# Optimization experiments

Hardware: AMD Instinct MI355X
Metric: run time of the kernel (lower is better)

The kernel has to match this reference:

```python
import jax, jax.numpy as jnp
import numpy as np

KERNEL_SIZES = [1, 2, 3]
KERNEL_NUM = 11
SIGMA = 0.1
EXACT_SIGMA = 0.001
EMBED_DIM = 300
HIDDEN = 128
Q_VOCAB = 30000
D_VOCAB = 30000


def _mus_sigmas():
    mus, sigmas = [], []
    K = KERNEL_NUM
    for i in range(K):
        mu = 1.0 / (K - 1) + 2.0 * i / (K - 1) - 1.0
        sigma = SIGMA
        if mu > 1.0:
            sigma = EXACT_SIGMA
            mu = 1.0
        mus.append(mu)
        sigmas.append(sigma)
    return jnp.asarray(mus, jnp.float32), jnp.asarray(sigmas, jnp.float32)


def _conv_tanh(x_bcl, w, b, ks):
    # x_bcl: (B, C_in, L); ConstantPad1d((0, ks)) + Conv1d(kernel=ks+1) keeps length L
    y = jax.lax.conv_general_dilated(
        x_bcl, w, window_strides=(1,), padding=[(0, ks)],
        dimension_numbers=('NCW', 'OIW', 'NCW'))
    return jnp.tanh(y + b[None, :, None])  # (B, H, L)


def _l2norm(x):
    n = jnp.sqrt(jnp.sum(x * x, axis=-1, keepdims=True))
    return x / jnp.maximum(n, 1e-12)


def setup_inputs() -> dict:
    key = jax.random.key(0)
    ks = jax.random.split(key, 16)
    inp = {
        'query': jax.random.randint(ks[0], (128, 128), 0, Q_VOCAB),
        'doc': jax.random.randint(ks[1], (128, 512), 0, D_VOCAB),
        'q_emb': jax.random.normal(ks[2], (Q_VOCAB, EMBED_DIM), jnp.float32) * 0.1,
        'd_emb': jax.random.normal(ks[3], (D_VOCAB, EMBED_DIM), jnp.float32) * 0.1,
        'out_w': jax.random.normal(ks[4], (1, 3 * 3 * KERNEL_NUM), jnp.float32) * 0.1,
        'out_b': jnp.zeros((1,), jnp.float32),
    }
    for idx, k in enumerate(KERNEL_SIZES):
        fan_in = EMBED_DIM * (k + 1)
        inp[f'conv_w{idx}'] = jax.random.normal(ks[5 + 2 * idx], (HIDDEN, EMBED_DIM, k + 1), jnp.float32) / np.sqrt(fan_in)
        inp[f'conv_b{idx}'] = jnp.zeros((HIDDEN,), jnp.float32)
    return inp


def reference(query, doc, q_emb, d_emb, conv_w0, conv_b0, conv_w1, conv_b1,
              conv_w2, conv_b2, out_w, out_b):
    mus, sigmas = _mus_sigmas()
    inv2s2 = 1.0 / (2.0 * sigmas * sigmas)  # (K,)

    q_e = q_emb[query].transpose(0, 2, 1)  # (B, D, Lq)
    d_e = d_emb[doc].transpose(0, 2, 1)    # (B, D, Ld)

    cws = [(conv_w0, conv_b0), (conv_w1, conv_b1), (conv_w2, conv_b2)]
    # q_convs/d_convs share weights (same nn.Sequential appended to both lists)
    q_convs = [_l2norm(_conv_tanh(q_e, w, b, ks).transpose(0, 2, 1))
               for (w, b), ks in zip(cws, KERNEL_SIZES)]  # each (B, Lq, H)
    d_convs = [_l2norm(_conv_tanh(d_e, w, b, ks).transpose(0, 2, 1))
               for (w, b), ks in zip(cws, KERNEL_SIZES)]  # each (B, Ld, H)

    KM = []
    for qi in range(3):
        for di in range(3):
            mm = jnp.einsum('bld,brd->blr', q_convs[qi], d_convs[di])  # (B,Lq,Ld)
            # Gaussian kernel soft-histogram, vectorized over all kernels
            kern = jnp.exp(-(mm[..., None] - mus) ** 2 * inv2s2)  # (B,Lq,Ld,K)
            K = jnp.log1p(kern.sum(axis=2)).sum(axis=1)           # (B,K)
            KM.append(K)
    phi = jnp.concatenate(KM, axis=1)  # (B, 9*KERNEL_NUM)
    return phi @ out_w.T + out_b       # (B, 1)
```

## Files before the change

### kernel.cpp

```cpp
#include <hip/hip_runtime.h>
#include <hip/hip_bf16.h>

typedef __hip_bfloat16 bf16;
typedef __attribute__((ext_vector_type(8))) short short8;
typedef __attribute__((ext_vector_type(4))) float f32x4;
typedef __attribute__((ext_vector_type(2))) float f32x2;

#define NB 128
#define NH 128
#define NLQ 128
#define NLD 512
#define NEMB 300
#define XQROWS 132
#define XDROWS 516
#define XCOLS 320

__device__ __forceinline__ unsigned short bfbits(float x) {
    __hip_bfloat16 h = __float2bfloat16(x);
    return *reinterpret_cast<unsigned short*>(&h);
}

__device__ __forceinline__ float fast_tanh(float x) {
    x = fminf(9.f, fmaxf(-9.f, x));
    float e = __builtin_amdgcn_exp2f(x * 2.8853900817779268f);
    return (e - 1.f) * __builtin_amdgcn_rcpf(e + 1.f);
}

__global__ void pack_w(const float* __restrict__ cw0, const float* __restrict__ cw1,
                       const float* __restrict__ cw2, bf16* __restrict__ Wp)
{
    int widx = blockIdx.y;
    int W = widx + 2;
    int e = blockIdx.x * 256 + threadIdx.x;
    if (e >= W * 40960) return;
    int ch = e >> 12;
    int cc = ch / W;
    int t  = ch - cc * W;
    int h  = (e >> 5) & 127;
    int cp = e & 31;
    int c  = cc * 32 + cp;
    const float* cw = (widx == 0) ? cw0 : (widx == 1 ? cw1 : cw2);
    float v = (c < NEMB) ? cw[(h * NEMB + c) * W + t] : 0.f;
    size_t off = (widx == 0) ? 0 : (widx == 1 ? 81920 : 204800);
    Wp[off + e] = __float2bfloat16(v);
}

__global__ __launch_bounds__(256)
void pack_x(const int* __restrict__ q_tok, const int* __restrict__ d_tok,
            const float* __restrict__ q_emb, const float* __restrict__ d_emb,
            bf16* __restrict__ Xq, bf16* __restrict__ Xd)
{
    int gid = blockIdx.x * 256 + threadIdx.x;
    int row = gid / 20, g = gid - row * 20;
    const float* emb; bf16* dst; int tok;
    if (row < NB * XQROWS) {
        int b = row / XQROWS, l = row - b * XQROWS;
        tok = (l < NLQ) ? q_tok[b * NLQ + l] : -1;
        emb = q_emb;
        dst = Xq + (size_t)row * XCOLS + g * 16;
    } else {
        int rowd = row - NB * XQROWS;
        int b = rowd / XDROWS, l = rowd - b * XDROWS;
        tok = (l < NLD) ? d_tok[b * NLD + l] : -1;
        emb = d_emb;
        dst = Xd + (size_t)rowd * XCOLS + g * 16;
    }
    int c0 = g * 16;
    float4 v[4];
    #pragma unroll
    for (int q = 0; q < 4; ++q) {
        int c = c0 + q * 4;
        v[q] = make_float4(0.f, 0.f, 0.f, 0.f);
        if (tok >= 0 && c < NEMB)
            v[q] = *reinterpret_cast<const float4*>(emb + (size_t)tok * NEMB + c);
    }
    short8 o0, o1;
    o0[0] = (short)bfbits(v[0].x); o0[1] = (short)bfbits(v[0].y);
    o0[2] = (short)bfbits(v[0].z); o0[3] = (short)bfbits(v[0].w);
    o0[4] = (short)bfbits(v[1].x); o0[5] = (short)bfbits(v[1].y);
    o0[6] = (short)bfbits(v[1].z); o0[7] = (short)bfbits(v[1].w);
    o1[0] = (short)bfbits(v[2].x); o1[1] = (short)bfbits(v[2].y);
    o1[2] = (short)bfbits(v[2].z); o1[3] = (short)bfbits(v[2].w);
    o1[4] = (short)bfbits(v[3].x); o1[5] = (short)bfbits(v[3].y);
    o1[6] = (short)bfbits(v[3].z); o1[7] = (short)bfbits(v[3].w);
    *reinterpret_cast<short8*>(dst) = o0;
    *reinterpret_cast<short8*>(dst + 8) = o1;
}

__global__ __launch_bounds__(512, 4)
void conv_kernel(const bf16* __restrict__ Xq, const bf16* __restrict__ Xd,
                 const bf16* __restrict__ Wp,
                 const float* __restrict__ cb0, const float* __restrict__ cb1,
                 const float* __restrict__ cb2,
                 bf16* __restrict__ qn, bf16* __restrict__ dn)
{
    __shared__ bf16 Xs[2][132][40];
    __shared__ float ssq[2][256];

    int bx = blockIdx.x;
    int widx = bx % 3;
    int inner = bx / 3;
    int W = widx + 2;
    const bf16* wp = Wp + ((widx == 0) ? 0 : (widx == 1 ? 81920 : 204800));
    const float* cb = (widx == 0) ? cb0 : (widx == 1 ? cb1 : cb2);

    int tid = threadIdx.x;
    int lane = tid & 63;
    int wv = tid >> 6;
    int wr = wv >> 1;
    int wc = wv & 1;
    int s_wave = wr >> 1;
    int lr_base = (wr & 1) * 64;

    bf16* outp; int L;
    int sb0, sb1, sl00, sl01;
    const bf16* xbase;
    size_t grow0, grow1;
    if (inner < 64) {
        outp = qn + (size_t)widx * NB * NLQ * NH;
        L = NLQ; sb0 = inner * 2; sb1 = sb0 + 1; sl00 = 0; sl01 = 0;
        xbase = Xq; grow0 = (size_t)sb0 * XQROWS; grow1 = (size_t)sb1 * XQROWS;
    } else {
        int i = inner - 64;
        outp = dn + (size_t)widx * NB * NLD * NH;
        L = NLD; sb0 = i >> 1; sb1 = sb0; sl00 = (i & 1) * 256; sl01 = sl00 + 128;
        xbase = Xd; grow0 = (size_t)sb0 * XDROWS + sl00; grow1 = grow0 + 128;
    }

    int sr = tid >> 2;
    int colg = tid & 3;
    const bf16* gsrc0 = xbase + (grow0 + sr) * XCOLS + colg * 8;
    const bf16* gsrc1 = xbase + (grow1 + sr) * XCOLS + colg * 8;
    bf16* ld0 = &Xs[0][sr][colg * 8];
    bf16* ld1 = &Xs[1][sr][colg * 8];
    bool has_tail = (tid >= 448 && tid < 480);
    int j = tid - 448;
    int ts = (j >> 2) >> 2, trr = 128 + ((j >> 2) & 3), tcolg = j & 3;
    const bf16* gsrcT = xbase + ((ts ? grow1 : grow0) + trr) * XCOLS + tcolg * 8;
    bf16* ldT = &Xs[ts][trr][tcolg * 8];

    short8 a0, a1, at;
    a0 = *reinterpret_cast<const short8*>(gsrc0);
    a1 = *reinterpret_cast<const short8*>(gsrc1);
    if (has_tail) at = *reinterpret_cast<const short8*>(gsrcT);
    *reinterpret_cast<short8*>(ld0) = a0;
    *reinterpret_cast<short8*>(ld1) = a1;
    if (has_tail) *reinterpret_cast<short8*>(ldT) = at;
    __syncthreads();

    f32x4 acc[4][4];
    #pragma unroll
    for (int m = 0; m < 4; ++m)
        #pragma unroll
        for (int n = 0; n < 4; ++n)
            acc[m][n] = (f32x4){0.f, 0.f, 0.f, 0.f};

    const bf16* pB = wp + ((size_t)((wc * 64 + (lane & 15)) * 4 + (lane >> 4))) * 8;

    int step = 0;
    for (int cc = 0; cc < 10; ++cc) {
        if (cc < 9) {
            a0 = *reinterpret_cast<const short8*>(gsrc0 + (cc + 1) * 32);
            a1 = *reinterpret_cast<const short8*>(gsrc1 + (cc + 1) * 32);
            if (has_tail) at = *reinterpret_cast<const short8*>(gsrcT + (cc + 1) * 32);
        }
        for (int t = 0; t < W; ++t, ++step) {
            const bf16* pBs = pB + (size_t)step * 4096;
            short8 bv[4], af[4];
            #pragma unroll
            for (int n = 0; n < 4; ++n)
                bv[n] = *reinterpret_cast<const short8*>(pBs + n * 512);
            #pragma unroll
            for (int m = 0; m < 4; ++m)
                af[m] = *reinterpret_cast<const short8*>(
                    &Xs[s_wave][lr_base + m * 16 + (lane & 15) + t][(lane >> 4) * 8]);
            #pragma unroll
            for (int m = 0; m < 4; ++m)
                #pragma unroll
                for (int n = 0; n < 4; ++n)
                    acc[m][n] = __builtin_amdgcn_mfma_f32_16x16x32_bf16(af[m], bv[n], acc[m][n], 0, 0, 0);
        }
        if (cc < 9) {
            __syncthreads();
            *reinterpret_cast<short8*>(ld0) = a0;
            *reinterpret_cast<short8*>(ld1) = a1;
            if (has_tail) *reinterpret_cast<short8*>(ldT) = at;
            __syncthreads();
        }
    }

    float ssl[4][4];
    #pragma unroll
    for (int m = 0; m < 4; ++m)
        #pragma unroll
        for (int i = 0; i < 4; ++i) ssl[m][i] = 0.f;

    #pragma unroll
    for (int n = 0; n < 4; ++n) {
        float bias = cb[wc * 64 + n * 16 + (lane & 15)];
        #pragma unroll
        for (int m = 0; m < 4; ++m)
            #pragma unroll
            for (int i = 0; i < 4; ++i) {
                float v = fast_tanh(acc[m][n][i] + bias);
                acc[m][n][i] = v;
                ssl[m][i] += v * v;
            }
    }
    #pragma unroll
    for (int m = 0; m < 4; ++m)
        #pragma unroll
        for (int i = 0; i < 4; ++i) {
            float s = ssl[m][i];
            s += __shfl_xor(s, 1); s += __shfl_xor(s, 2);
            s += __shfl_xor(s, 4); s += __shfl_xor(s, 8);
            ssl[m][i] = s;
        }
    if ((lane & 15) == 0) {
        #pragma unroll
        for (int m = 0; m < 4; ++m)
            #pragma unroll
            for (int i = 0; i < 4; ++i)
                ssq[wc][wr * 64 + m * 16 + (lane >> 4) * 4 + i] = ssl[m][i];
    }
    __syncthreads();
    #pragma unroll
    for (int m = 0; m < 4; ++m)
        #pragma unroll
        for (int i = 0; i < 4; ++i) {
            int r = wr * 64 + m * 16 + (lane >> 4) * 4 + i;
            float s2 = ssq[0][r] + ssq[1][r];
            float sc = 1.f / fmaxf(sqrtf(s2), 1e-12f);
            int s = r >> 7, lr = r & 127;
            int b = s ? sb1 : sb0;
            int l = (s ? sl01 : sl00) + lr;
            bf16* dst = outp + ((size_t)(b * L + l)) * NH;
            #pragma unroll
            for (int n = 0; n < 4; ++n)
                dst[wc * 64 + n * 16 + (lane & 15)] = __float2bfloat16(acc[m][n][i] * sc);
        }
}

__global__ __launch_bounds__(512, 4)
void sim_kernel(const bf16* __restrict__ qn, const bf16* __restrict__ dn,
                float* __restrict__ phi)
{
    __shared__ bf16 Qs[128][136];
    __shared__ bf16 Ds[64][136];
    __shared__ float wsum[2][11];
    float (*red)[128][11] = reinterpret_cast<float(*)[128][11]>(&Ds[0][0]);

    int blk = blockIdx.x;
    int b = blk / 9;
    int pair = blk - b * 9;
    int qi = pair / 3, di = pair - qi * 3;

    int tid = threadIdx.x, lane = tid & 63, wv = tid >> 6;
    int wr = wv >> 2;
    int wc = wv & 3;

    const bf16* qbase = qn + ((size_t)qi * NB + b) * (NLQ * NH);
    const bf16* dbase = dn + ((size_t)di * NB + b) * (NLD * NH);

    {
        int r = tid >> 2, h0 = (tid & 3) * 32;
        #pragma unroll
        for (int v = 0; v < 4; ++v)
            *reinterpret_cast<short8*>(&Qs[r][h0 + v * 8]) =
                *reinterpret_cast<const short8*>(qbase + (size_t)r * NH + h0 + v * 8);
    }

    int dr = tid >> 3, dc = (tid & 7) * 16;
    {
        short8 st[2];
        #pragma unroll
        for (int v = 0; v < 2; ++v)
            st[v] = *reinterpret_cast<const short8*>(dbase + (size_t)dr * NH + dc + v * 8);
        #pragma unroll
        for (int v = 0; v < 2; ++v)
            *reinterpret_cast<short8*>(&Ds[dr][dc + v * 8]) = st[v];
    }
    __syncthreads();

    f32x2 sums2[2][11];
    #pragma unroll
    for (int n = 0; n < 2; ++n)
        #pragma unroll
        for (int k = 0; k < 11; ++k) sums2[n][k] = (f32x2){0.f, 0.f};

    const float C1 = 1.8315638888734179e-2f;
    const float C2 = 3.3546262790251185e-4f;
    const float C3 = 6.1442123533282098e-6f;
    const float C4 = 1.1253517471925912e-7f;

    for (int cc = 0; cc < 8; ++cc) {
        f32x4 acc[2][2];
        #pragma unroll
        for (int m = 0; m < 2; ++m)
            #pragma unroll
            for (int n = 0; n < 2; ++n)
                acc[m][n] = (f32x4){0.f, 0.f, 0.f, 0.f};

        #pragma unroll
        for (int kc = 0; kc < 4; ++kc) {
            short8 af[2], bq[2];
            #pragma unroll
            for (int m = 0; m < 2; ++m)
                af[m] = *reinterpret_cast<const short8*>(
                    &Ds[wr * 32 + m * 16 + (lane & 15)][kc * 32 + (lane >> 4) * 8]);
            #pragma unroll
            for (int n = 0; n < 2; ++n)
                bq[n] = *reinterpret_cast<const short8*>(
                    &Qs[wc * 32 + n * 16 + (lane & 15)][kc * 32 + (lane >> 4) * 8]);
            #pragma unroll
            for (int m = 0; m < 2; ++m)
                #pragma unroll
                for (int n = 0; n < 2; ++n)
                    acc[m][n] = __builtin_amdgcn_mfma_f32_16x16x32_bf16(af[m], bq[n], acc[m][n], 0, 0, 0);
        }
        __syncthreads();

        short8 st[2];
        if (cc < 7) {
            #pragma unroll
            for (int v = 0; v < 2; ++v)
                st[v] = *reinterpret_cast<const short8*>(
                    dbase + (size_t)((cc + 1) * 64 + dr) * NH + dc + v * 8);
        }

        #pragma unroll
        for (int n = 0; n < 2; ++n)
            #pragma unroll
            for (int i = 0; i < 4; ++i) {
                f32x2 x2;
                x2.x = acc[0][n][i];
                x2.y = acc[1][n][i];
                f32x2 ax = x2 * 28.853900817779268f;
                f32x2 R, Ri, E4;
                R.x = __builtin_amdgcn_exp2f(ax.x);
                R.y = __builtin_amdgcn_exp2f(ax.y);
                Ri.x = __builtin_amdgcn_rcpf(R.x);
                Ri.y = __builtin_amdgcn_rcpf(R.y);
                f32x2 d4 = x2 + 0.1f;
                f32x2 t = d4 * d4 * (-72.134752044448169f);
                E4.x = __builtin_amdgcn_exp2f(t.x);
                E4.y = __builtin_amdgcn_exp2f(t.y);
                sums2[n][4] += E4;
                f32x2 u = E4 * R;
                sums2[n][5] += u;
                u *= R; u *= C1; sums2[n][6] += u;
                u *= R; u *= C2; sums2[n][7] += u;
                u *= R; u *= C3; sums2[n][8] += u;
                u *= R; u *= C4; sums2[n][9] += u;
                f32x2 w = E4 * Ri; w *= C1; sums2[n][3] += w;
                w *= Ri; w *= C2; sums2[n][2] += w;
                w *= Ri; w *= C3; sums2[n][1] += w;
                w *= Ri; w *= C4; sums2[n][0] += w;
                if (__any(fmaxf(x2.x, x2.y) > 0.98f)) {
                    f32x2 d1 = x2 - 1.0f;
                    f32x2 t1 = d1 * d1 * (-721347.52044448f);
                    f32x2 e;
                    e.x = __builtin_amdgcn_exp2f(t1.x);
                    e.y = __builtin_amdgcn_exp2f(t1.y);
                    sums2[n][10] += e;
                }
            }

        if (cc < 7) {
            #pragma unroll
            for (int v = 0; v < 2; ++v)
                *reinterpret_cast<short8*>(&Ds[dr][dc + v * 8]) = st[v];
            __syncthreads();
        }
    }

    #pragma unroll
    for (int n = 0; n < 2; ++n)
        #pragma unroll
        for (int k = 0; k < 11; ++k) {
            float s = sums2[n][k].x + sums2[n][k].y;
            s += __shfl_xor(s, 16);
            s += __shfl_xor(s, 32);
            sums2[n][k].x = s;
        }
    if ((lane >> 4) == 0) {
        #pragma unroll
        for (int n = 0; n < 2; ++n)
            #pragma unroll
            for (int k = 0; k < 11; ++k)
                red[wr][wc * 32 + n * 16 + (lane & 15)][k] = sums2[n][k].x;
    }
    __syncthreads();
    if (tid < 128) {
        float lv[11];
        #pragma unroll
        for (int k = 0; k < 11; ++k)
            lv[k] = log1pf(red[0][tid][k] + red[1][tid][k]);
        #pragma unroll
        for (int k = 0; k < 11; ++k) {
            float s = lv[k];
            s += __shfl_xor(s, 1); s += __shfl_xor(s, 2); s += __shfl_xor(s, 4);
            s += __shfl_xor(s, 8); s += __shfl_xor(s, 16); s += __shfl_xor(s, 32);
            lv[k] = s;
        }
        if ((tid & 63) == 0) {
            #pragma unroll
            for (int k = 0; k < 11; ++k) wsum[tid >> 6][k] = lv[k];
        }
    }
    __syncthreads();
    if (tid < 11) phi[b * 99 + pair * 11 + tid] = wsum[0][tid] + wsum[1][tid];
}

__global__ void final_kernel(const float* __restrict__ phi, const float* __restrict__ ow,
                             const float* __restrict__ obias, float* __restrict__ out)
{
    int b = threadIdx.x;
    float s = obias[0];
    #pragma unroll
    for (int j = 0; j < 99; ++j) s += phi[b * 99 + j] * ow[j];
    out[b] = s;
}

extern "C" void kernel_launch(void* const* d_in, const int* in_sizes, int n_in,
                              void* d_out, int out_size, void* d_ws, size_t ws_size,
                              hipStream_t stream)
{
    const int*   query = (const int*)d_in[0];
    const int*   doc   = (const int*)d_in[1];
    const float* q_emb = (const float*)d_in[2];
    const float* d_emb = (const float*)d_in[3];
    const float* out_w = (const float*)d_in[4];
    const float* out_b = (const float*)d_in[5];
    const float* cw0 = (const float*)d_in[6];
    const float* cb0 = (const float*)d_in[7];
    const float* cw1 = (const float*)d_in[8];
    const float* cb1 = (const float*)d_in[9];
    const float* cw2 = (const float*)d_in[10];
    const float* cb2 = (const float*)d_in[11];

    const size_t QN = (size_t)NB * NLQ * NH;
    const size_t DN = (size_t)NB * NLD * NH;
    const size_t XQN = (size_t)NB * XQROWS * XCOLS;
    const size_t XDN = (size_t)NB * XDROWS * XCOLS;

    bf16* Wp = (bf16*)d_ws;
    bf16* Xq = Wp + 368640;
    bf16* Xd = Xq + XQN;
    bf16* qn = Xd + XDN;
    bf16* dn = qn + 3 * QN;
    float* phi = (float*)(dn + 3 * DN);

    pack_w<<<dim3(640, 3), 256, 0, stream>>>(cw0, cw1, cw2, Wp);
    pack_x<<<6480, 256, 0, stream>>>(query, doc, q_emb, d_emb, Xq, Xd);
    conv_kernel<<<960, 512, 0, stream>>>(Xq, Xd, Wp, cb0, cb1, cb2, qn, dn);
    sim_kernel<<<NB * 9, 512, 0, stream>>>(qn, dn, phi);
    final_kernel<<<1, 128, 0, stream>>>(phi, out_w, out_b, (float*)d_out);
}
```

Measured before the change: 227.9 us.

## Double-buffer conv LDS tile and template conv body on kernel width

The conv kernel now keeps two LDS buffers for the input tile, so the next chunk is written into the alternate buffer and only one barrier per chunk is needed instead of two. The body is also templated on the window width, which lets the inner tap loop fully unroll with compile-time weight offsets. The cost is doubled LDS per block, which may lower the number of resident blocks per CU. An extra barrier protects the ssq reduction buffer.

```diff
diff --git a/kernel.cpp b/kernel.cpp
--- a/kernel.cpp
+++ b/kernel.cpp
@@ -87,23 +87,13 @@
     *reinterpret_cast<short8*>(dst + 8) = o1;
 }
 
-__global__ __launch_bounds__(512, 4)
-void conv_kernel(const bf16* __restrict__ Xq, const bf16* __restrict__ Xd,
-                 const bf16* __restrict__ Wp,
-                 const float* __restrict__ cb0, const float* __restrict__ cb1,
-                 const float* __restrict__ cb2,
-                 bf16* __restrict__ qn, bf16* __restrict__ dn)
-{
-    __shared__ bf16 Xs[2][132][40];
-    __shared__ float ssq[2][256];
-
-    int bx = blockIdx.x;
-    int widx = bx % 3;
-    int inner = bx / 3;
-    int W = widx + 2;
-    const bf16* wp = Wp + ((widx == 0) ? 0 : (widx == 1 ? 81920 : 204800));
-    const float* cb = (widx == 0) ? cb0 : (widx == 1 ? cb1 : cb2);
-
+template<int W>
+__device__ __forceinline__ void conv_body(
+    const bf16* __restrict__ Xq, const bf16* __restrict__ Xd,
+    const bf16* __restrict__ wp, const float* __restrict__ cb,
+    bf16* __restrict__ qn_w, bf16* __restrict__ dn_w,
+    int inner, bf16 Xs[2][2][132][40], float ssq[2][256])
+{
     int tid = threadIdx.x;
     int lane = tid & 63;
     int wv = tid >> 6;
@@ -117,12 +107,12 @@
     const bf16* xbase;
     size_t grow0, grow1;
     if (inner < 64) {
-        outp = qn + (size_t)widx * NB * NLQ * NH;
+        outp = qn_w;
         L = NLQ; sb0 = inner * 2; sb1 = sb0 + 1; sl00 = 0; sl01 = 0;
         xbase = Xq; grow0 = (size_t)sb0 * XQROWS; grow1 = (size_t)sb1 * XQROWS;
     } else {
         int i = inner - 64;
-        outp = dn + (size_t)widx * NB * NLD * NH;
+        outp = dn_w;
         L = NLD; sb0 = i >> 1; sb1 = sb0; sl00 = (i & 1) * 256; sl01 = sl00 + 128;
         xbase = Xd; grow0 = (size_t)sb0 * XDROWS + sl00; grow1 = grow0 + 128;
     }
@@ -131,21 +121,20 @@
     int colg = tid & 3;
     const bf16* gsrc0 = xbase + (grow0 + sr) * XCOLS + colg * 8;
     const bf16* gsrc1 = xbase + (grow1 + sr) * XCOLS + colg * 8;
-    bf16* ld0 = &Xs[0][sr][colg * 8];
-    bf16* ld1 = &Xs[1][sr][colg * 8];
     bool has_tail = (tid >= 448 && tid < 480);
     int j = tid - 448;
     int ts = (j >> 2) >> 2, trr = 128 + ((j >> 2) & 3), tcolg = j & 3;
     const bf16* gsrcT = xbase + ((ts ? grow1 : grow0) + trr) * XCOLS + tcolg * 8;
-    bf16* ldT = &Xs[ts][trr][tcolg * 8];
-
-    short8 a0, a1, at;
-    a0 = *reinterpret_cast<const short8*>(gsrc0);
-    a1 = *reinterpret_cast<const short8*>(gsrc1);
-    if (has_tail) at = *reinterpret_cast<const short8*>(gsrcT);
-    *reinterpret_cast<short8*>(ld0) = a0;
-    *reinterpret_cast<short8*>(ld1) = a1;
-    if (has_tail) *reinterpret_cast<short8*>(ldT) = at;
+
+    {
+        short8 a0 = *reinterpret_cast<const short8*>(gsrc0);
+        short8 a1 = *reinterpret_cast<const short8*>(gsrc1);
+        short8 at;
+        if (has_tail) at = *reinterpret_cast<const short8*>(gsrcT);
+        *reinterpret_cast<short8*>(&Xs[0][0][sr][colg * 8]) = a0;
+        *reinterpret_cast<short8*>(&Xs[0][1][sr][colg * 8]) = a1;
+        if (has_tail) *reinterpret_cast<short8*>(&Xs[0][ts][trr][tcolg * 8]) = at;
+    }
     __syncthreads();
 
     f32x4 acc[4][4];
@@ -157,15 +146,17 @@
 
     const bf16* pB = wp + ((size_t)((wc * 64 + (lane & 15)) * 4 + (lane >> 4))) * 8;
 
-    int step = 0;
+    int cur = 0;
     for (int cc = 0; cc < 10; ++cc) {
+        short8 a0n, a1n, atn;
         if (cc < 9) {
-            a0 = *reinterpret_cast<const short8*>(gsrc0 + (cc + 1) * 32);
-            a1 = *reinterpret_cast<const short8*>(gsrc1 + (cc + 1) * 32);
-            if (has_tail) at = *reinterpret_cast<const short8*>(gsrcT + (cc + 1) * 32);
-        }
-        for (int t = 0; t < W; ++t, ++step) {
-            const bf16* pBs = pB + (size_t)step * 4096;
+            a0n = *reinterpret_cast<const short8*>(gsrc0 + (cc + 1) * 32);
+            a1n = *reinterpret_cast<const short8*>(gsrc1 + (cc + 1) * 32);
+            if (has_tail) atn = *reinterpret_cast<const short8*>(gsrcT + (cc + 1) * 32);
+        }
+        #pragma unroll
+        for (int t = 0; t < W; ++t) {
+            const bf16* pBs = pB + (size_t)(cc * W + t) * 4096;
             short8 bv[4], af[4];
             #pragma unroll
             for (int n = 0; n < 4; ++n)
@@ -173,7 +164,7 @@
             #pragma unroll
             for (int m = 0; m < 4; ++m)
                 af[m] = *reinterpret_cast<const short8*>(
-                    &Xs[s_wave][lr_base + m * 16 + (lane & 15) + t][(lane >> 4) * 8]);
+                    &Xs[cur][s_wave][lr_base + m * 16 + (lane & 15) + t][(lane >> 4) * 8]);
             #pragma unroll
             for (int m = 0; m < 4; ++m)
                 #pragma unroll
@@ -181,12 +172,12 @@
                     acc[m][n] = __builtin_amdgcn_mfma_f32_16x16x32_bf16(af[m], bv[n], acc[m][n], 0, 0, 0);
         }
         if (cc < 9) {
+            *reinterpret_cast<short8*>(&Xs[cur ^ 1][0][sr][colg * 8]) = a0n;
+            *reinterpret_cast<short8*>(&Xs[cur ^ 1][1][sr][colg * 8]) = a1n;
+            if (has_tail) *reinterpret_cast<short8*>(&Xs[cur ^ 1][ts][trr][tcolg * 8]) = atn;
             __syncthreads();
-            *reinterpret_cast<short8*>(ld0) = a0;
-            *reinterpret_cast<short8*>(ld1) = a1;
-            if (has_tail) *reinterpret_cast<short8*>(ldT) = at;
-            __syncthreads();
-        }
+        }
+        cur ^= 1;
     }
 
     float ssl[4][4];
@@ -216,6 +207,7 @@
             s += __shfl_xor(s, 4); s += __shfl_xor(s, 8);
             ssl[m][i] = s;
         }
+    __syncthreads();
     if ((lane & 15) == 0) {
         #pragma unroll
         for (int m = 0; m < 4; ++m)
@@ -239,6 +231,28 @@
             for (int n = 0; n < 4; ++n)
                 dst[wc * 64 + n * 16 + (lane & 15)] = __float2bfloat16(acc[m][n][i] * sc);
         }
+}
+
+__global__ __launch_bounds__(512, 4)
+void conv_kernel(const bf16* __restrict__ Xq, const bf16* __restrict__ Xd,
+                 const bf16* __restrict__ Wp,
+                 const float* __restrict__ cb0, const float* __restrict__ cb1,
+                 const float* __restrict__ cb2,
+                 bf16* __restrict__ qn, bf16* __restrict__ dn)
+{
+    __shared__ bf16 Xs[2][2][132][40];
+    __shared__ float ssq[2][256];
+    const size_t QN = (size_t)NB * NLQ * NH;
+    const size_t DN = (size_t)NB * NLD * NH;
+
+    int widx = blockIdx.x % 3;
+    int inner = blockIdx.x / 3;
+    if (widx == 0)
+        conv_body<2>(Xq, Xd, Wp, cb0, qn, dn, inner, Xs, ssq);
+    else if (widx == 1)
+        conv_body<3>(Xq, Xd, Wp + 81920, cb1, qn + QN, dn + DN, inner, Xs, ssq);
+    else
+        conv_body<4>(Xq, Xd, Wp + 204800, cb2, qn + 2 * QN, dn + 2 * DN, inner, Xs, ssq);
 }
 
 __global__ __launch_bounds__(512, 4)
```

After: 253.0 us. +11.0%, slower.

## Merge packing kernels and double-buffer conv LDS tiles to drop a barrier

Applied to the files above, without the earlier changes.

Merges the weight-packing and embedding-gather kernels into one launch, with the first 1440 blocks packing weights and the rest gathering embeddings, which removes one kernel launch and its gap. In the conv kernel the shared X tile is now double-buffered: the next chunk is written to the alternate buffer right after compute, so each chunk step needs one barrier instead of two. The cost is twice the LDS for the X tile (about 42KB), which may reduce how many 512-thread blocks fit per CU.

```diff
diff --git a/kernel.cpp b/kernel.cpp
--- a/kernel.cpp
+++ b/kernel.cpp
@@ -26,31 +26,32 @@
     return (e - 1.f) * __builtin_amdgcn_rcpf(e + 1.f);
 }
 
-__global__ void pack_w(const float* __restrict__ cw0, const float* __restrict__ cw1,
-                       const float* __restrict__ cw2, bf16* __restrict__ Wp)
+__global__ __launch_bounds__(256)
+void pack_all(const int* __restrict__ q_tok, const int* __restrict__ d_tok,
+              const float* __restrict__ q_emb, const float* __restrict__ d_emb,
+              const float* __restrict__ cw0, const float* __restrict__ cw1,
+              const float* __restrict__ cw2,
+              bf16* __restrict__ Wp, bf16* __restrict__ Xq, bf16* __restrict__ Xd)
 {
-    int widx = blockIdx.y;
-    int W = widx + 2;
-    int e = blockIdx.x * 256 + threadIdx.x;
-    if (e >= W * 40960) return;
-    int ch = e >> 12;
-    int cc = ch / W;
-    int t  = ch - cc * W;
-    int h  = (e >> 5) & 127;
-    int cp = e & 31;
-    int c  = cc * 32 + cp;
-    const float* cw = (widx == 0) ? cw0 : (widx == 1 ? cw1 : cw2);
-    float v = (c < NEMB) ? cw[(h * NEMB + c) * W + t] : 0.f;
-    size_t off = (widx == 0) ? 0 : (widx == 1 ? 81920 : 204800);
-    Wp[off + e] = __float2bfloat16(v);
-}
-
-__global__ __launch_bounds__(256)
-void pack_x(const int* __restrict__ q_tok, const int* __restrict__ d_tok,
-            const float* __restrict__ q_emb, const float* __restrict__ d_emb,
-            bf16* __restrict__ Xq, bf16* __restrict__ Xd)
-{
-    int gid = blockIdx.x * 256 + threadIdx.x;
+    int bx = blockIdx.x;
+    if (bx < 1440) {
+        int e = bx * 256 + threadIdx.x;
+        int widx = (e >= 204800) ? 2 : (e >= 81920 ? 1 : 0);
+        int off = (widx == 0) ? 0 : (widx == 1 ? 81920 : 204800);
+        int el = e - off;
+        int W = widx + 2;
+        int ch = el >> 12;
+        int cc = ch / W;
+        int t  = ch - cc * W;
+        int h  = (el >> 5) & 127;
+        int cp = el & 31;
+        int c  = cc * 32 + cp;
+        const float* cw = (widx == 0) ? cw0 : (widx == 1 ? cw1 : cw2);
+        float v = (c < NEMB) ? cw[(h * NEMB + c) * W + t] : 0.f;
+        Wp[e] = __float2bfloat16(v);
+        return;
+    }
+    int gid = (bx - 1440) * 256 + threadIdx.x;
     int row = gid / 20, g = gid - row * 20;
     const float* emb; bf16* dst; int tok;
     if (row < NB * XQROWS) {
@@ -94,7 +95,7 @@
                  const float* __restrict__ cb2,
                  bf16* __restrict__ qn, bf16* __restrict__ dn)
 {
-    __shared__ bf16 Xs[2][132][40];
+    __shared__ bf16 Xs[2][2][132][40];
     __shared__ float ssq[2][256];
 
     int bx = blockIdx.x;
@@ -131,21 +132,18 @@
     int colg = tid & 3;
     const bf16* gsrc0 = xbase + (grow0 + sr) * XCOLS + colg * 8;
     const bf16* gsrc1 = xbase + (grow1 + sr) * XCOLS + colg * 8;
-    bf16* ld0 = &Xs[0][sr][colg * 8];
-    bf16* ld1 = &Xs[1][sr][colg * 8];
     bool has_tail = (tid >= 448 && tid < 480);
     int j = tid - 448;
     int ts = (j >> 2) >> 2, trr = 128 + ((j >> 2) & 3), tcolg = j & 3;
     const bf16* gsrcT = xbase + ((ts ? grow1 : grow0) + trr) * XCOLS + tcolg * 8;
-    bf16* ldT = &Xs[ts][trr][tcolg * 8];
 
     short8 a0, a1, at;
     a0 = *reinterpret_cast<const short8*>(gsrc0);
     a1 = *reinterpret_cast<const short8*>(gsrc1);
     if (has_tail) at = *reinterpret_cast<const short8*>(gsrcT);
-    *reinterpret_cast<short8*>(ld0) = a0;
-    *reinterpret_cast<short8*>(ld1) = a1;
-    if (has_tail) *reinterpret_cast<short8*>(ldT) = at;
+    *reinterpret_cast<short8*>(&Xs[0][0][sr][colg * 8]) = a0;
+    *reinterpret_cast<short8*>(&Xs[0][1][sr][colg * 8]) = a1;
+    if (has_tail) *reinterpret_cast<short8*>(&Xs[0][ts][trr][tcolg * 8]) = at;
     __syncthreads();
 
     f32x4 acc[4][4];
@@ -157,7 +155,7 @@
 
     const bf16* pB = wp + ((size_t)((wc * 64 + (lane & 15)) * 4 + (lane >> 4))) * 8;
 
-    int step = 0;
+    int cur = 0, step = 0;
     for (int cc = 0; cc < 10; ++cc) {
         if (cc < 9) {
             a0 = *reinterpret_cast<const short8*>(gsrc0 + (cc + 1) * 32);
@@ -173,7 +171,7 @@
             #pragma unroll
             for (int m = 0; m < 4; ++m)
                 af[m] = *reinterpret_cast<const short8*>(
-                    &Xs[s_wave][lr_base + m * 16 + (lane & 15) + t][(lane >> 4) * 8]);
+                    &Xs[cur][s_wave][lr_base + m * 16 + (lane & 15) + t][(lane >> 4) * 8]);
             #pragma unroll
             for (int m = 0; m < 4; ++m)
                 #pragma unroll
@@ -181,11 +179,11 @@
                     acc[m][n] = __builtin_amdgcn_mfma_f32_16x16x32_bf16(af[m], bv[n], acc[m][n], 0, 0, 0);
         }
         if (cc < 9) {
+            *reinterpret_cast<short8*>(&Xs[cur ^ 1][0][sr][colg * 8]) = a0;
+            *reinterpret_cast<short8*>(&Xs[cur ^ 1][1][sr][colg * 8]) = a1;
+            if (has_tail) *reinterpret_cast<short8*>(&Xs[cur ^ 1][ts][trr][tcolg * 8]) = at;
             __syncthreads();
-            *reinterpret_cast<short8*>(ld0) = a0;
-            *reinterpret_cast<short8*>(ld1) = a1;
-            if (has_tail) *reinterpret_cast<short8*>(ldT) = at;
-            __syncthreads();
+            cur ^= 1;
         }
     }
 
@@ -451,8 +449,7 @@
     bf16* dn = qn + 3 * QN;
     float* phi = (float*)(dn + 3 * DN);
 
-    pack_w<<<dim3(640, 3), 256, 0, stream>>>(cw0, cw1, cw2, Wp);
-    pack_x<<<6480, 256, 0, stream>>>(query, doc, q_emb, d_emb, Xq, Xd);
+    pack_all<<<7920, 256, 0, stream>>>(query, doc, q_emb, d_emb, cw0, cw1, cw2, Wp, Xq, Xd);
     conv_kernel<<<960, 512, 0, stream>>>(Xq, Xd, Wp, cb0, cb1, cb2, qn, dn);
     sim_kernel<<<NB * 9, 512, 0, stream>>>(qn, dn, phi);
     final_kernel<<<1, 128, 0, stream>>>(phi, out_w, out_b, (float*)d_out);
```

Result: faster. 219.6 us (-3.7%).
